# Performance work log

Measured on AMD Instinct MI355X. Metric: run time of the kernel, lower is better.

## Reference

```python
import jax, jax.numpy as jnp
import numpy as np

V = 16000      # vocab_size
D = 256        # embedding_dim
H = 512        # hidden_size (bi-LSTM concat)
HD = H // 2    # per-direction hidden
LAB = 32       # labelset_size (30 tags + START/STOP)
T = 512        # seq length
B = 128        # batch
START = 30
STOP = 31
NEG = -10000.0


def setup_inputs() -> dict:
    key = jax.random.key(0)
    ks = jax.random.split(key, 16)
    sc = 0.05
    emb = jax.random.normal(ks[0], (V, D), jnp.float32) * 0.1
    W_ih_f = jax.random.normal(ks[1], (4 * HD, D), jnp.float32) * sc
    W_hh_f = jax.random.normal(ks[2], (4 * HD, HD), jnp.float32) * sc
    b_f = jax.random.normal(ks[3], (4 * HD,), jnp.float32) * sc  # b_ih + b_hh combined
    W_ih_b = jax.random.normal(ks[4], (4 * HD, D), jnp.float32) * sc
    W_hh_b = jax.random.normal(ks[5], (4 * HD, HD), jnp.float32) * sc
    b_b = jax.random.normal(ks[6], (4 * HD,), jnp.float32) * sc
    Wo = jax.random.normal(ks[7], (LAB, H), jnp.float32) * sc
    bo = jnp.zeros((LAB,), jnp.float32)
    transitions = jax.random.normal(ks[8], (LAB, LAB), jnp.float32)
    transitions = transitions.at[STOP, :].set(NEG).at[:, START].set(NEG)
    h0 = jax.random.normal(ks[9], (2, B, HD), jnp.float32)  # init_hidden() uses randn
    c0 = jax.random.normal(ks[10], (2, B, HD), jnp.float32)
    sentences = jax.random.randint(ks[11], (T, B), 0, V, dtype=jnp.int32)
    labels = jax.random.randint(ks[12], (T, B), 0, 30, dtype=jnp.int32)
    masks = jnp.ones((T, B), dtype=bool)
    return {"emb": emb, "W_ih_f": W_ih_f, "W_hh_f": W_hh_f, "b_f": b_f,
            "W_ih_b": W_ih_b, "W_hh_b": W_hh_b, "b_b": b_b,
            "Wo": Wo, "bo": bo, "transitions": transitions,
            "h0": h0, "c0": c0,
            "sentences": sentences, "labels": labels, "masks": masks}


def _lstm_dir(xproj, h0, c0, W_hh):
    # xproj: [T, B, 4*HD] precomputed input projection (+bias)
    def step(carry, xg):
        h, c = carry
        g = xg + h @ W_hh.T
        i, f, gg, o = jnp.split(g, 4, axis=-1)  # torch gate order i,f,g,o
        i = jax.nn.sigmoid(i); f = jax.nn.sigmoid(f)
        gg = jnp.tanh(gg); o = jax.nn.sigmoid(o)
        c = f * c + i * gg
        h = o * jnp.tanh(c)
        return (h, c), h
    _, hs = jax.lax.scan(step, (h0, c0), xproj)
    return hs  # [T, B, HD]


def reference(emb, W_ih_f, W_hh_f, b_f, W_ih_b, W_hh_b, b_b, Wo, bo,
              transitions, h0, c0, sentences, labels, masks):
    # ---- encoder (dropout omitted: eval-mode determinism) ----
    x = emb[sentences]                                   # [T, B, D]
    xf = jnp.einsum('tbd,gd->tbg', x, W_ih_f) + b_f
    hf = _lstm_dir(xf, h0[0], c0[0], W_hh_f)             # [T, B, HD]
    xb = jnp.einsum('tbd,gd->tbg', x, W_ih_b) + b_b
    hb = _lstm_dir(xb[::-1], h0[1], c0[1], W_hh_b)[::-1]
    out = jnp.concatenate([hf, hb], axis=-1)             # [T, B, H]
    feats = jnp.einsum('tbh,lh->tbl', out, Wo) + bo      # [T, B, LAB]

    # ---- CRF forward algorithm (log partition) ----
    dp0 = jnp.full((B, LAB), NEG, jnp.float32).at[:, START].set(0.0)
    def fstep(dp, inp):
        sc, m = inp  # sc: [B, LAB], m: [B]
        new = jax.scipy.special.logsumexp(
            dp[:, :, None] + transitions[None, :, :] + sc[:, None, :], axis=1)
        return jnp.where(m[:, None], new, dp), None
    dpZ, _ = jax.lax.scan(fstep, dp0, (feats, masks))
    Z = jax.scipy.special.logsumexp(dpZ, axis=1)         # [B]

    # ---- gold path score ----
    lab_ext = jnp.concatenate(
        [jnp.full((1, B), START, labels.dtype), labels], axis=0)  # [T+1, B]
    bidx = jnp.arange(B)
    def gstep(dp, inp):
        sc, m, lp, ln = inp
        tmp = dp + transitions[lp, ln] + sc[bidx, ln]
        return jnp.where(m, tmp, dp), None
    gold, _ = jax.lax.scan(gstep, jnp.zeros((B,), jnp.float32),
                           (feats, masks, lab_ext[:-1], lab_ext[1:]))

    return (Z - gold).sum() / B
```

## Files before the change

### kernel.cpp

```cpp
#include <hip/hip_runtime.h>
#include <stdint.h>

typedef __attribute__((ext_vector_type(8))) short short8;
typedef __attribute__((ext_vector_type(4))) float floatx4;
typedef __attribute__((ext_vector_type(8))) int intx8;
typedef __attribute__((ext_vector_type(2))) int intx2;
typedef unsigned int u32;
typedef unsigned short u16;
typedef unsigned long long u64;

#define NROW 65536
#define RING 32

#define OFF_TAGS  64
#define OFF_READY 256
#define OFF_WIH   8192
#define OFF_WHH8  1056768
#define OFF_WO    2105344
#define OFF_RING  2138112
#define OFF_OUT   19177472
#define OFF_FE    86286336
#define WS_NEED   94674944

__device__ __forceinline__ u16 f2bf(float f){
  union { float f; u32 u; } v; v.f = f;
  u32 u = v.u;
  return (u16)((u + 0x7FFFu + ((u >> 16) & 1u)) >> 16);
}
__device__ __forceinline__ float bf2f(u16 h){
  union { u32 u; float f; } v; v.u = ((u32)h) << 16; return v.f;
}
__device__ __forceinline__ u32 pack2(float a, float b){
  return (u32)f2bf(a) | ((u32)f2bf(b) << 16);
}
__device__ __forceinline__ u32 pk_fp8x4(float a, float b, float c, float d){
  u32 lo = __builtin_amdgcn_cvt_pk_fp8_f32(a, b, 0, false);
  return (u32)__builtin_amdgcn_cvt_pk_fp8_f32(c, d, lo, true);
}
__device__ __forceinline__ float sigm(float x){
  return __builtin_amdgcn_rcpf(1.f + __expf(-x));
}
__device__ __forceinline__ float tanh_(float x){
  return 1.f - 2.f * __builtin_amdgcn_rcpf(1.f + __expf(2.f * x));
}
__device__ __forceinline__ floatx4 MF(short8 a, short8 b, floatx4 c){
  return __builtin_amdgcn_mfma_f32_16x16x32_bf16(a, b, c, 0, 0, 0);
}
__device__ __forceinline__ floatx4 MFS(intx8 a, intx8 b, floatx4 c){
  return __builtin_amdgcn_mfma_scale_f32_16x16x128_f8f6f4(
      a, b, c, 0, 0, 0, 0x7F7F7F7F, 0, 0x7F7F7F7F);
}
template<int CTRL>
__device__ __forceinline__ u32 dppq(u32 x){
  return (u32)__builtin_amdgcn_update_dpp(0, (int)x, CTRL, 0xF, 0xF, false);
}
__device__ __forceinline__ void ldsload16(const void* g, void* l){
  __builtin_amdgcn_global_load_lds(
      (const __attribute__((address_space(1))) u32*)g,
      (__attribute__((address_space(3))) u32*)l, 16, 0, 17);
}

__global__ void kdiag(float* out, float v){
  if (threadIdx.x == 0 && blockIdx.x == 0) out[0] = v;
}

__global__ void k0(const float* wf, const float* wb, const float* hf, const float* hb,
                   const float* wo, u16* wih, u16* wob, unsigned char* whh8){
  int e = blockIdx.x * 256 + threadIdx.x;
  if (e < 524288){ wih[e] = f2bf(e < 262144 ? wf[e] : wb[e - 262144]); return; }
  if (e < 540672){ wob[e - 524288] = f2bf(wo[e - 524288]); return; }
  if (e < 1064960){
    int t = e - 540672;
    float w = (t < 262144) ? hf[t] : hb[t - 262144];
    whh8[t] = (unsigned char)(__builtin_amdgcn_cvt_pk_fp8_f32(w, w, 0, false) & 0xFF);
  }
}

__global__ void __launch_bounds__(1024) __attribute__((amdgpu_waves_per_eu(4, 4)))
klstm(const float* emb, const int* sent, const u16* wih,
      const float* bf_, const float* bb_,
      const unsigned char* whh8, const float* h0, const float* c0,
      char* ring, u16* outb, u32* ct, u32* ready){
  __shared__ __align__(16) char SH[98304];
  const int tid = threadIdx.x, w = tid >> 6, l = tid & 63, q = l >> 4, l15 = l & 15;
  const int bid = blockIdx.x;

  if (bid >= 32){
    const int pid = bid - 32, dir = pid & 1;
    const int rem = pid >> 1;
    const int j = rem >> 1;
    const int half = rem & 1;
    const float* bias = dir ? bb_ : bf_;
    const int m = w & 7, ch = w >> 3;
    int pbud = 1 << 20;
    for (int s = j; s < 512; s += 56){
      const int t = dir ? 511 - s : s;
      if (s >= 31){
        const int li = l, need = s - 30;
        bool done = false;
        while (!done && pbud > 0){
          int v = need;
          if (li < 16)
            v = (int)__hip_atomic_load(&ct[dir * 16 + li], __ATOMIC_RELAXED, __HIP_MEMORY_SCOPE_AGENT);
          done = (__ballot(v >= need) == ~0ull);
          if (!done){ __builtin_amdgcn_s_sleep(32); pbud--; }
        }
      }
      {
        int r = tid >> 3, g0 = tid & 7;
        const float* er = emb + (size_t)sent[t * 128 + r] * 256;
        #pragma unroll
        for (int jj = 0; jj < 4; jj++){
          int g8 = g0 + jj * 8;
          float4 a = *(const float4*)(er + g8 * 8);
          float4 b = *(const float4*)(er + g8 * 8 + 4);
          u32 gg[4] = { pack2(a.x, a.y), pack2(a.z, a.w), pack2(b.x, b.y), pack2(b.z, b.w) };
          *(uint4*)&SH[(g8 * 128 + r) * 16] = *(uint4*)gg;
        }
      }
      __syncthreads();
      short8 Afr[8];
      #pragma unroll
      for (int ks = 0; ks < 8; ks++)
        Afr[ks] = *(const short8*)&SH[((ks * 4 + q) * 128 + m * 16 + l15) * 16];
      char* slot = ring + (size_t)(dir * RING + (s & (RING - 1))) * 262144;
      const int bcw = m * 2 + (q >> 1);
      const int nt0 = half * 8;
      for (int nt = nt0; nt < nt0 + 8; nt++){
        __syncthreads();
        {
          #pragma unroll
          for (int pass = 0; pass < 2; pass++){
            int f = pass * 1024 + tid;
            int frag = f >> 6;
            int ks = frag >> 2, jt = (frag >> 1) & 1, fch = frag & 1;
            int lq = (f >> 4) & 3, fl = f & 15;
            int c = fch * 32 + jt * 16 + fl, kg = ks * 4 + lq;
            uint4 v = *(const uint4*)(wih + (size_t)(dir * 1024 + nt * 64 + c) * 256 + kg * 8);
            *(uint4*)&SH[65536 + f * 16] = v;
          }
        }
        __syncthreads();
        floatx4 acc[2];
        acc[0] = floatx4{0.f,0.f,0.f,0.f};
        acc[1] = floatx4{0.f,0.f,0.f,0.f};
        #pragma unroll
        for (int ks = 0; ks < 8; ks++){
          #pragma unroll
          for (int jt = 0; jt < 2; jt++){
            short8 b = *(const short8*)&SH[65536 + ((((ks * 2 + jt) * 2 + ch) * 64 + l) * 16)];
            acc[jt] = MF(Afr[ks], b, acc[jt]);
          }
        }
        #pragma unroll
        for (int jt = 0; jt < 2; jt++){
          int col = nt * 64 + ch * 32 + jt * 16 + l15;
          float bv = bias[col];
          u32 pr[2] = { pack2(acc[jt][0] + bv, acc[jt][1] + bv),
                        pack2(acc[jt][2] + bv, acc[jt][3] + bv) };
          *(uint2*)(slot + bcw * 16384 + col * 16 + (q & 1) * 8) = *(uint2*)pr;
        }
      }
      asm volatile("s_waitcnt vmcnt(0)" ::: "memory");
      __syncthreads();
      if (tid == 0){
        __builtin_amdgcn_fence(__ATOMIC_RELEASE, "agent");
        __hip_atomic_fetch_add(&ready[dir * 512 + s], 1u, __ATOMIC_RELAXED, __HIP_MEMORY_SCOPE_AGENT);
      }
    }
    return;
  }

  const int dir = bid >> 4, bc = bid & 15;
  const int nn = w >> 1, hw = w & 1;
  const int H0 = nn * 32 + hw * 16, hid = H0 + l15;
  const int b0loc = (q & 1) * 4 + (q >> 1) * 2;
  const int i4 = l15 & 3, j4 = l15 >> 2;
  int cbud = 1 << 22;
  const u32 s01 = i4==0?0x00000400u : i4==1?0x00000105u : i4==2?0x06020000u : 0x03070000u;
  const u32 s23 = i4==0?0x04000000u : i4==1?0x01050000u : i4==2?0x00000602u : 0x00000307u;
  const u32 sfn = (i4 < 2) ? 0x07060100u : 0x03020504u;

  intx8 Wf[4][2];
  #pragma unroll
  for (int g = 0; g < 4; g++){
    const unsigned char* wr = whh8 + (size_t)(dir * 1024 + g * 256 + hid) * 256;
    #pragma unroll
    for (int i = 0; i < 2; i++)
      Wf[g][i] = *(const intx8*)(wr + i * 128 + q * 32);
  }
  float creg[2];
  #pragma unroll
  for (int e = 0; e < 2; e++)
    creg[e] = c0[((size_t)dir * 128 + bc * 8 + b0loc + e) * 256 + hid];
  {
    int a = tid * 4;
    int kg = a >> 7, rest = a & 127, b = rest >> 3, off4 = a & 4;
    u32 val0 = 0;
    if (b < 8){
      const float* hr = h0 + ((size_t)dir * 128 + bc * 8 + b) * 256 + kg * 8 + off4;
      val0 = pk_fp8x4(hr[0], hr[1], hr[2], hr[3]);
    }
    *(u32*)&SH[65536 + a] = val0;
    *(u32*)&SH[65536 + 4096 + a] = 0;
  }
  #pragma unroll
  for (int pp = 0; pp < 3; pp++){
    while (__hip_atomic_load(&ready[dir * 512 + pp], __ATOMIC_RELAXED, __HIP_MEMORY_SCOPE_AGENT) < 2u
           && --cbud > 0)
      __builtin_amdgcn_s_sleep(8);
    const char* rp = ring + (size_t)(dir * RING + pp) * 262144 + bc * 16384;
    ldsload16(rp + tid * 16, SH + pp * 16384 + tid * 16);
  }
  u32 rdyv = __hip_atomic_load(&ready[dir * 512 + 3], __ATOMIC_RELAXED, __HIP_MEMORY_SCOPE_AGENT);
  asm volatile("s_waitcnt vmcnt(0)" ::: "memory");
  __syncthreads();

  for (int s = 0; s < 512; s++){
    const int t = dir ? 511 - s : s;
    u32 rdyn = 2u;
    if (s + 4 < 512)
      rdyn = __hip_atomic_load(&ready[dir * 512 + s + 4], __ATOMIC_RELAXED, __HIP_MEMORY_SCOPE_AGENT);
    if (s + 3 < 512){
      if (rdyv < 2u){
        while (__hip_atomic_load(&ready[dir * 512 + s + 3], __ATOMIC_RELAXED, __HIP_MEMORY_SCOPE_AGENT) < 2u
               && --cbud > 0)
          __builtin_amdgcn_s_sleep(2);
      }
      const char* rp = ring + (size_t)(dir * RING + ((s + 3) & (RING - 1))) * 262144 + bc * 16384;
      ldsload16(rp + tid * 16, SH + ((s + 3) & 3) * 16384 + tid * 16);
    }
    rdyv = rdyn;

    const char* xb0 = SH + (s & 3) * 16384;
    u32 xg[4];
    #pragma unroll
    for (int g = 0; g < 4; g++)
      xg[g] = *(const u32*)(xb0 + ((g * 256 + hid) * 16 + b0loc * 2));

    const char* hb = SH + 65536 + (s & 1) * 4096;
    floatx4 acc[4];
    #pragma unroll
    for (int g = 0; g < 4; g++) acc[g] = floatx4{0.f,0.f,0.f,0.f};
    #pragma unroll
    for (int i = 0; i < 2; i++){
      union { long l[4]; intx8 v; } au;
      #pragma unroll
      for (int jj = 0; jj < 4; jj++)
        au.l[jj] = *(const long*)(hb + ((i * 16 + q * 4 + jj) * 16 + l15) * 8);
      #pragma unroll
      for (int g = 0; g < 4; g++)
        acc[g] = MFS(au.v, Wf[g][i], acc[g]);
    }

    float v[4][2];
    #pragma unroll
    for (int g = 0; g < 4; g++)
      #pragma unroll
      for (int e = 0; e < 2; e++){
        union { float f; int i; } lo, hi;
        lo.f = acc[g][e]; hi.f = acc[g][2 + e];
        intx2 r = __builtin_amdgcn_permlane32_swap(lo.i, hi.i, false, false);
        union { int i; float f; } o; o.i = r[0];
        v[g][e] = o.f;
      }

    float hv[2];
    #pragma unroll
    for (int e = 0; e < 2; e++){
      float gi = v[0][e] + bf2f((u16)(xg[0] >> (16 * e)));
      float gf = v[1][e] + bf2f((u16)(xg[1] >> (16 * e)));
      float gg = v[2][e] + bf2f((u16)(xg[2] >> (16 * e)));
      float go = v[3][e] + bf2f((u16)(xg[3] >> (16 * e)));
      gi = sigm(gi); gf = sigm(gf); gg = tanh_(gg); go = sigm(go);
      float c = gf * creg[e] + gi * gg;
      creg[e] = c;
      hv[e] = go * tanh_(c);
      outb[((size_t)t * 128 + bc * 8 + b0loc + e) * 512 + dir * 256 + hid] = f2bf(hv[e]);
    }

    {
      u32 pk = (u32)__builtin_amdgcn_cvt_pk_fp8_f32(hv[0], hv[1], 0, false);
      intx2 rq = __builtin_amdgcn_permlane32_swap((int)pk, (int)pk, false, false);
      u32 quad = (u32)rq[0] | ((u32)rq[1] << 16);
      u32 r1 = dppq<0xB1>(quad);
      u32 r2 = dppq<0x4E>(quad);
      u32 r3 = dppq<0x1B>(quad);
      u32 p01 = __builtin_amdgcn_perm(r1, quad, s01);
      u32 p23 = __builtin_amdgcn_perm(r3, r2, s23);
      u32 outw = __builtin_amdgcn_perm(p23, p01, sfn);
      char* hn = SH + 65536 + ((s + 1) & 1) * 4096;
      if (q < 2){
        int bq = q * 4 + i4;
        int hidg = H0 + j4 * 4;
        *(u32*)&hn[(hidg >> 3) * 128 + bq * 8 + (hidg & 4)] = outw;
      }
    }
    if (tid == 0)
      __hip_atomic_store(&ct[dir * 16 + bc], (u32)(s + 1), __ATOMIC_RELAXED, __HIP_MEMORY_SCOPE_AGENT);

    if (s < 508){
      asm volatile("s_waitcnt vmcnt(10) lgkmcnt(0)" ::: "memory");
      __builtin_amdgcn_s_barrier();
    } else if (s < 511){
      asm volatile("s_waitcnt vmcnt(0)" ::: "memory");
      __syncthreads();
    }
  }
}

__launch_bounds__(256, 2)
__global__ void k5(const u16* outb, const u16* wob, const float* bo, float* fe){
  const int tid = threadIdx.x, w = tid >> 6, l15 = tid & 15, q = (tid >> 4) & 3;
  const int rows0 = blockIdx.x * 64;
  short8 WoF[2][16];
  #pragma unroll
  for (int jt = 0; jt < 2; jt++)
    #pragma unroll
    for (int ks = 0; ks < 16; ks++)
      WoF[jt][ks] = *(const short8*)(wob + (size_t)(jt * 16 + l15) * 512 + ks * 32 + q * 8);
  floatx4 a5[2] = { floatx4{0.f,0.f,0.f,0.f}, floatx4{0.f,0.f,0.f,0.f} };
  const u16* ar = outb + (size_t)(rows0 + w * 16 + l15) * 512;
  #pragma unroll
  for (int ks = 0; ks < 16; ks++){
    short8 a = *(const short8*)(ar + ks * 32 + q * 8);
    a5[0] = MF(a, WoF[0][ks], a5[0]);
    a5[1] = MF(a, WoF[1][ks], a5[1]);
  }
  #pragma unroll
  for (int jt = 0; jt < 2; jt++){
    float bv = bo[jt * 16 + l15];
    #pragma unroll
    for (int rg = 0; rg < 4; rg++)
      fe[(size_t)(rows0 + w * 16 + q * 4 + rg) * 32 + jt * 16 + l15] = a5[jt][rg] + bv;
  }
}

__global__ void k6(const float* fe, const int* labels, const float* trans, float* accp){
  __shared__ float TrL[1024];
  __shared__ __align__(16) float dpL[4][32];
  const int tid = threadIdx.x, w = tid >> 6, l = tid & 63, j = l & 31, half = l >> 5;
  const int b = blockIdx.x * 4 + w;
  for (int i = tid; i < 1024; i += 256) TrL[i] = trans[i];
  __syncthreads();
  float Trl[16];
  #pragma unroll
  for (int ii = 0; ii < 16; ii++) Trl[ii] = TrL[(half * 16 + ii) * 32 + j];
  if (half == 0) dpL[w][j] = (j == 30) ? 0.f : -10000.f;

  float gold = 0.f; int lp = 30;
  float sc = fe[(size_t)b * 32 + j];
  int lab = labels[b];
  float ndF = 0.f;
  for (int t = 0; t < 512; t++){
    float scN = 0.f; int labN = 0;
    if (t < 511){
      scN = fe[((size_t)(t + 1) * 128 + b) * 32 + j];
      labN = labels[(t + 1) * 128 + b];
    }
    float dpv[16], tt[16];
    {
      const float4 a = *(const float4*)&dpL[w][half * 16 + 0];
      const float4 b4 = *(const float4*)&dpL[w][half * 16 + 4];
      const float4 c4 = *(const float4*)&dpL[w][half * 16 + 8];
      const float4 d4 = *(const float4*)&dpL[w][half * 16 + 12];
      dpv[0]=a.x; dpv[1]=a.y; dpv[2]=a.z; dpv[3]=a.w;
      dpv[4]=b4.x; dpv[5]=b4.y; dpv[6]=b4.z; dpv[7]=b4.w;
      dpv[8]=c4.x; dpv[9]=c4.y; dpv[10]=c4.z; dpv[11]=c4.w;
      dpv[12]=d4.x; dpv[13]=d4.y; dpv[14]=d4.z; dpv[15]=d4.w;
    }
    float m = -3.0e38f;
    #pragma unroll
    for (int ii = 0; ii < 16; ii++){ tt[ii] = dpv[ii] + Trl[ii]; m = fmaxf(m, tt[ii]); }
    float M = fmaxf(m, __shfl_xor(m, 32));
    float ssum = 0.f;
    #pragma unroll
    for (int ii = 0; ii < 16; ii++) ssum += __expf(tt[ii] - M);
    ssum += __shfl_xor(ssum, 32);
    float nd = sc + M + __logf(ssum);
    float scl = __shfl(sc, lab);
    gold += TrL[lp * 32 + lab] + scl;
    lp = lab;
    if (half == 0) dpL[w][j] = nd;
    ndF = nd;
    sc = scN; lab = labN;
  }
  float M2 = ndF, S2 = 1.f;
  #pragma unroll
  for (int off = 1; off < 64; off <<= 1){
    float Mo = __shfl_xor(M2, off), So = __shfl_xor(S2, off);
    float Mn = fmaxf(M2, Mo);
    S2 = S2 * __expf(M2 - Mn) + So * __expf(Mo - Mn);
    M2 = Mn;
  }
  float Z = M2 + __logf(S2 * 0.5f);
  if (l == 0) atomicAdd(accp, Z - gold);
}

__global__ void k7(const float* accp, float* out){
  if (threadIdx.x == 0 && blockIdx.x == 0) out[0] = accp[0] * (1.f / 128.f);
}

extern "C" void kernel_launch(void* const* d_in, const int* in_sizes, int n_in,
                              void* d_out, int out_size, void* d_ws, size_t ws_size,
                              hipStream_t stream){
  float* outp = (float*)d_out;
  if (ws_size < (size_t)WS_NEED){
    hipLaunchKernelGGL(kdiag, dim3(1), dim3(64), 0, stream, outp, (float)ws_size);
    return;
  }
  const float* emb  = (const float*)d_in[0];
  const float* Wihf = (const float*)d_in[1];
  const float* Whhf = (const float*)d_in[2];
  const float* bf_  = (const float*)d_in[3];
  const float* Wihb = (const float*)d_in[4];
  const float* Whhb = (const float*)d_in[5];
  const float* bb_  = (const float*)d_in[6];
  const float* Wo   = (const float*)d_in[7];
  const float* bo   = (const float*)d_in[8];
  const float* trans= (const float*)d_in[9];
  const float* h0   = (const float*)d_in[10];
  const float* c0   = (const float*)d_in[11];
  const int*   sent = (const int*)d_in[12];
  const int*   labels = (const int*)d_in[13];

  char* ws = (char*)d_ws;
  float* accp = (float*)ws;
  u32* ct    = (u32*)(ws + OFF_TAGS);
  u32* ready = (u32*)(ws + OFF_READY);
  u16* wih   = (u16*)(ws + OFF_WIH);
  unsigned char* whh8 = (unsigned char*)(ws + OFF_WHH8);
  u16* wob   = (u16*)(ws + OFF_WO);
  char* ring = ws + OFF_RING;
  u16* outb  = (u16*)(ws + OFF_OUT);
  float* fe  = (float*)(ws + OFF_FE);

  hipMemsetAsync(d_ws, 0, 8192, stream);
  hipLaunchKernelGGL(k0, dim3(4160), dim3(256), 0, stream,
                     Wihf, Wihb, Whhf, Whhb, Wo, wih, wob, whh8);
  hipLaunchKernelGGL(klstm, dim3(256), dim3(1024), 0, stream,
                     emb, sent, wih, bf_, bb_, whh8, h0, c0, ring, outb, ct, ready);
  hipLaunchKernelGGL(k5, dim3(1024), dim3(256), 0, stream, outb, wob, bo, fe);
  hipLaunchKernelGGL(k6, dim3(32), dim3(256), 0, stream, fe, labels, trans, accp);
  hipLaunchKernelGGL(k7, dim3(1), dim3(64), 0, stream, accp, outp);
}
```

Measured before the change: 1.307 ms.

## Keep CRF forward state in registers using DPP and permlane exchanges

Rewrites the CRF forward-recurrence kernel so the per-step dp vector is exchanged across lanes with permlane16/32 swaps and DPP row rotations instead of an LDS write/read each step. Transition values are pre-rotated per lane to match the rotation pattern, and the max/exp sums are reduced in tree form. It also prefetches emissions two steps ahead and computes the gold score with scalar readlane. The goal is to shorten the serial 512-step dependency chain; the cost is reliance on gfx950-specific builtins, with an LDS fallback when they are missing.

Measured after the change: 1.351 ms. 1.03x slower.

```diff
diff --git a/kernel.cpp b/kernel.cpp
--- a/kernel.cpp
+++ b/kernel.cpp
@@ -22,6 +22,12 @@
 #define OFF_FE    86286336
 #define WS_NEED   94674944
 
+#if __has_builtin(__builtin_amdgcn_permlane16_swap)
+#define HAVE_PL16 1
+#else
+#define HAVE_PL16 0
+#endif
+
 __device__ __forceinline__ u16 f2bf(float f){
   union { float f; u32 u; } v; v.f = f;
   u32 u = v.u;
@@ -54,10 +60,29 @@
 __device__ __forceinline__ u32 dppq(u32 x){
   return (u32)__builtin_amdgcn_update_dpp(0, (int)x, CTRL, 0xF, 0xF, false);
 }
+template<int R>
+__device__ __forceinline__ float rowror(float x){
+  union { float f; int i; } u; u.f = x;
+  union { int i; float f; } o;
+  o.i = __builtin_amdgcn_update_dpp(0, u.i, 0x120 | R, 0xF, 0xF, false);
+  return o.f;
+}
+__device__ __forceinline__ float plane32partner(float x, bool lowhalf){
+  union { float f; int i; } u; u.f = x;
+  intx2 r = __builtin_amdgcn_permlane32_swap(u.i, u.i, false, false);
+  union { int i; float f; } a, b; a.i = r[0]; b.i = r[1];
+  return lowhalf ? b.f : a.f;
+}
 __device__ __forceinline__ void ldsload16(const void* g, void* l){
   __builtin_amdgcn_global_load_lds(
       (const __attribute__((address_space(1))) u32*)g,
       (__attribute__((address_space(3))) u32*)l, 16, 0, 17);
+}
+__device__ __forceinline__ float rdlane(float v, int lane){
+  union { float f; int i; } u; u.f = v;
+  union { int i; float f; } o;
+  o.i = __builtin_amdgcn_readlane(u.i, lane);
+  return o.f;
 }
 
 __global__ void kdiag(float* out, float v){
@@ -336,56 +361,89 @@
   }
 }
 
+__launch_bounds__(256)
 __global__ void k6(const float* fe, const int* labels, const float* trans, float* accp){
   __shared__ float TrL[1024];
-  __shared__ __align__(16) float dpL[4][32];
-  const int tid = threadIdx.x, w = tid >> 6, l = tid & 63, j = l & 31, half = l >> 5;
+  __shared__ float dpw[4][32];
+  const int tid = threadIdx.x, w = tid >> 6, l = tid & 63, j = l & 31, p = l & 15;
+  const int row = l >> 4;
+  const int h = (row == 1 || row == 2) ? 1 : 0;
+  const bool lowhalf = (l < 32);
   const int b = blockIdx.x * 4 + w;
   for (int i = tid; i < 1024; i += 256) TrL[i] = trans[i];
   __syncthreads();
-  float Trl[16];
-  #pragma unroll
-  for (int ii = 0; ii < 16; ii++) Trl[ii] = TrL[(half * 16 + ii) * 32 + j];
-  if (half == 0) dpL[w][j] = (j == 30) ? 0.f : -10000.f;
-
+  float Trr[16];
+  #pragma unroll
+  for (int r = 0; r < 16; r++) Trr[r] = TrL[(h * 16 + ((p + r) & 15)) * 32 + j];
+
+  float nd = (j == 30) ? 0.f : -10000.f;
   float gold = 0.f; int lp = 30;
-  float sc = fe[(size_t)b * 32 + j];
-  int lab = labels[b];
-  float ndF = 0.f;
+  float sc  = fe[(size_t)b * 32 + j];
+  float sc1 = fe[(size_t)(128 + b) * 32 + j];
+  int lab  = labels[b];
+  int lab1 = labels[128 + b];
+
   for (int t = 0; t < 512; t++){
-    float scN = 0.f; int labN = 0;
-    if (t < 511){
-      scN = fe[((size_t)(t + 1) * 128 + b) * 32 + j];
-      labN = labels[(t + 1) * 128 + b];
-    }
-    float dpv[16], tt[16];
+    float sc2 = 0.f; int lab2 = 0;
+    if (t + 2 < 512){
+      sc2 = fe[((size_t)(t + 2) * 128 + b) * 32 + j];
+      lab2 = labels[(t + 2) * 128 + b];
+    }
+    int slab = __builtin_amdgcn_readfirstlane(lab);
+    gold += TrL[lp * 32 + slab] + rdlane(sc, slab);
+    lp = slab;
+
+    float dpr;
+#if HAVE_PL16
     {
-      const float4 a = *(const float4*)&dpL[w][half * 16 + 0];
-      const float4 b4 = *(const float4*)&dpL[w][half * 16 + 4];
-      const float4 c4 = *(const float4*)&dpL[w][half * 16 + 8];
-      const float4 d4 = *(const float4*)&dpL[w][half * 16 + 12];
-      dpv[0]=a.x; dpv[1]=a.y; dpv[2]=a.z; dpv[3]=a.w;
-      dpv[4]=b4.x; dpv[5]=b4.y; dpv[6]=b4.z; dpv[7]=b4.w;
-      dpv[8]=c4.x; dpv[9]=c4.y; dpv[10]=c4.z; dpv[11]=c4.w;
-      dpv[12]=d4.x; dpv[13]=d4.y; dpv[14]=d4.z; dpv[15]=d4.w;
-    }
-    float m = -3.0e38f;
-    #pragma unroll
-    for (int ii = 0; ii < 16; ii++){ tt[ii] = dpv[ii] + Trl[ii]; m = fmaxf(m, tt[ii]); }
-    float M = fmaxf(m, __shfl_xor(m, 32));
-    float ssum = 0.f;
-    #pragma unroll
-    for (int ii = 0; ii < 16; ii++) ssum += __expf(tt[ii] - M);
-    ssum += __shfl_xor(ssum, 32);
-    float nd = sc + M + __logf(ssum);
-    float scl = __shfl(sc, lab);
-    gold += TrL[lp * 32 + lab] + scl;
-    lp = lab;
-    if (half == 0) dpL[w][j] = nd;
-    ndF = nd;
-    sc = scN; lab = labN;
-  }
-  float M2 = ndF, S2 = 1.f;
+      union { float f; int i; } u; u.f = nd;
+      intx2 pr = __builtin_amdgcn_permlane16_swap(u.i, u.i, false, false);
+      union { int i; float f; } o0, o1; o0.i = pr[0]; o1.i = pr[1];
+      dpr = (h == 0) ? o0.f : o1.f;
+    }
+#else
+    if (lowhalf) dpw[w][j] = nd;
+    dpr = dpw[w][h * 16 + p];
+#endif
+
+    float tt[16];
+    tt[0]  = dpr            + Trr[0];
+    tt[1]  = rowror<1>(dpr)  + Trr[1];
+    tt[2]  = rowror<2>(dpr)  + Trr[2];
+    tt[3]  = rowror<3>(dpr)  + Trr[3];
+    tt[4]  = rowror<4>(dpr)  + Trr[4];
+    tt[5]  = rowror<5>(dpr)  + Trr[5];
+    tt[6]  = rowror<6>(dpr)  + Trr[6];
+    tt[7]  = rowror<7>(dpr)  + Trr[7];
+    tt[8]  = rowror<8>(dpr)  + Trr[8];
+    tt[9]  = rowror<9>(dpr)  + Trr[9];
+    tt[10] = rowror<10>(dpr) + Trr[10];
+    tt[11] = rowror<11>(dpr) + Trr[11];
+    tt[12] = rowror<12>(dpr) + Trr[12];
+    tt[13] = rowror<13>(dpr) + Trr[13];
+    tt[14] = rowror<14>(dpr) + Trr[14];
+    tt[15] = rowror<15>(dpr) + Trr[15];
+    float f0 = fmaxf(tt[0], tt[1]),  f1 = fmaxf(tt[2], tt[3]);
+    float f2 = fmaxf(tt[4], tt[5]),  f3 = fmaxf(tt[6], tt[7]);
+    float f4 = fmaxf(tt[8], tt[9]),  f5 = fmaxf(tt[10], tt[11]);
+    float f6 = fmaxf(tt[12], tt[13]), f7 = fmaxf(tt[14], tt[15]);
+    float g0 = fmaxf(f0, f1), g1 = fmaxf(f2, f3), g2 = fmaxf(f4, f5), g3 = fmaxf(f6, f7);
+    float m = fmaxf(fmaxf(g0, g1), fmaxf(g2, g3));
+    float Mt = fmaxf(m, plane32partner(m, lowhalf));
+    float e0 = __expf(tt[0] - Mt) + __expf(tt[1] - Mt);
+    float e1 = __expf(tt[2] - Mt) + __expf(tt[3] - Mt);
+    float e2 = __expf(tt[4] - Mt) + __expf(tt[5] - Mt);
+    float e3 = __expf(tt[6] - Mt) + __expf(tt[7] - Mt);
+    float e4 = __expf(tt[8] - Mt) + __expf(tt[9] - Mt);
+    float e5 = __expf(tt[10] - Mt) + __expf(tt[11] - Mt);
+    float e6 = __expf(tt[12] - Mt) + __expf(tt[13] - Mt);
+    float e7 = __expf(tt[14] - Mt) + __expf(tt[15] - Mt);
+    float s = ((e0 + e1) + (e2 + e3)) + ((e4 + e5) + (e6 + e7));
+    float stot = s + plane32partner(s, lowhalf);
+    nd = sc + Mt + __logf(stot);
+    sc = sc1; sc1 = sc2; lab = lab1; lab1 = lab2;
+  }
+  float M2 = nd, S2 = 1.f;
   #pragma unroll
   for (int off = 1; off < 64; off <<= 1){
     float Mo = __shfl_xor(M2, off), So = __shfl_xor(S2, off);
```
